# Optimization experiments

Measured on AMD Instinct MI355X. Metric: run time of the kernel, lower is better.

Reference implementation:

```python
import jax, jax.numpy as jnp
import numpy as np

B_, L_, OBS = 16, 1024, 64
H, NB, NST, DC, EXP = 256, 4, 16, 4, 2
DIN = EXP * H          # 512
DTR = (H + 15) // 16   # dt_rank = 16


def setup_inputs() -> dict:
    key = jax.random.key(0)
    ks = jax.random.split(key, 12)
    s = 0.02
    A_log = jnp.tile(jnp.log(jnp.arange(1, NST + 1, dtype=jnp.float32)), (NB, DIN, 1))
    return {
        "x": jax.random.normal(ks[0], (B_, L_, OBS), jnp.float32),
        "proj_w": jax.random.normal(ks[1], (H, OBS), jnp.float32) * s,
        "proj_b": jnp.zeros((H,), jnp.float32),
        "in_proj_w": jax.random.normal(ks[2], (NB, 2 * DIN, H), jnp.float32) * s,
        "conv_w": jax.random.normal(ks[3], (NB, DIN, DC), jnp.float32) * s,
        "conv_b": jnp.zeros((NB, DIN), jnp.float32),
        "x_proj_w": jax.random.normal(ks[4], (NB, DTR + 2 * NST, DIN), jnp.float32) * s,
        "dt_proj_w": jax.random.normal(ks[5], (NB, DIN, DTR), jnp.float32) * s,
        "dt_proj_b": jax.random.normal(ks[6], (NB, DIN), jnp.float32) * 0.1 - 3.0,
        "A_log": A_log,
        "D_skip": jnp.ones((NB, DIN), jnp.float32),
        "out_proj_w": jax.random.normal(ks[7], (NB, H, DIN), jnp.float32) * s,
        "head_w": jax.random.normal(ks[8], (1, H), jnp.float32) * s,
        "head_b": jnp.zeros((1,), jnp.float32),
    }


def _mamba(x, ipw, cw, cb, xpw, dpw, dpb, Alog, Dsk, opw):
    # x: [B, L, H]
    Bb, L, _ = x.shape
    xz = jnp.einsum('blh,eh->ble', x, ipw)           # [B,L,2*DIN]
    xin, z = jnp.split(xz, 2, axis=-1)
    # causal depthwise conv1d
    xc = jnp.transpose(xin, (0, 2, 1))               # [B,DIN,L]
    xc = jax.lax.conv_general_dilated(
        xc, cw[:, None, :], (1,), [(DC - 1, 0)],
        dimension_numbers=('NCH', 'OIH', 'NCH'), feature_group_count=DIN)
    u = jax.nn.silu(jnp.transpose(xc + cb[None, :, None], (0, 2, 1)))  # [B,L,DIN]
    # input-dependent dt, B, C
    proj = jnp.einsum('bld,ed->ble', u, xpw)         # [B,L,DTR+2*NST]
    dtl, Bc, Cc = jnp.split(proj, [DTR, DTR + NST], axis=-1)
    dt = jax.nn.softplus(jnp.einsum('blr,dr->bld', dtl, dpw) + dpb)     # [B,L,DIN]
    A = -jnp.exp(Alog)                               # [DIN,NST]

    def step(h, t):
        dt_t, B_t, C_t, u_t = t                      # [B,DIN],[B,NST],[B,NST],[B,DIN]
        h = jnp.exp(dt_t[:, :, None] * A) * h + (dt_t * u_t)[:, :, None] * B_t[:, None, :]
        return h, jnp.einsum('bdn,bn->bd', h, C_t)

    seq = (jnp.moveaxis(dt, 1, 0), jnp.moveaxis(Bc, 1, 0),
           jnp.moveaxis(Cc, 1, 0), jnp.moveaxis(u, 1, 0))
    h0 = jnp.zeros((Bb, DIN, NST), x.dtype)
    _, ys = jax.lax.scan(step, h0, seq)              # [L,B,DIN]
    y = jnp.moveaxis(ys, 0, 1) + Dsk * u
    y = y * jax.nn.silu(z)
    return jnp.einsum('bld,hd->blh', y, opw)


def reference(x, proj_w, proj_b, in_proj_w, conv_w, conv_b, x_proj_w,
              dt_proj_w, dt_proj_b, A_log, D_skip, out_proj_w, head_w, head_b):
    h = jnp.einsum('blo,ho->blh', x, proj_w) + proj_b
    for i in range(NB):
        h = _mamba(h, in_proj_w[i], conv_w[i], conv_b[i], x_proj_w[i],
                   dt_proj_w[i], dt_proj_b[i], A_log[i], D_skip[i], out_proj_w[i])
    v = jnp.einsum('bh,oh->bo', h[:, -1, :], head_w) + head_b  # [B,1]
    return v.squeeze(-1)
```

## Files before the change

### kernel.cpp

```cpp
#include <hip/hip_runtime.h>
#include <cstddef>

#define Bb 16
#define Ll 1024
#define OBS 64
#define Hh 256
#define NBLK 4
#define NST 16
#define DCV 4
#define DIN 512
#define DTR 16
#define NC 32
#define CL (Ll / NC)

typedef short short8 __attribute__((ext_vector_type(8)));
typedef float f32x4 __attribute__((ext_vector_type(4)));

#define LOG2E 1.4426950408889634f

#define HSZ ((size_t)Bb * Ll * Hh)
static const size_t OFF_XIN  = 2 * HSZ;
static const size_t OFF_Z    = OFF_XIN + (size_t)Bb * Ll * DIN;
static const size_t OFF_U    = OFF_Z   + (size_t)Bb * Ll * DIN;
static const size_t OFF_PROJ = OFF_U   + (size_t)Bb * Ll * DIN;
static const size_t OFF_HST  = OFF_PROJ + (size_t)Bb * Ll * 48;
static const size_t OFF_SDT  = OFF_HST + (size_t)Bb * NC * NST * DIN;
static const size_t OFF_WC   = OFF_SDT + (size_t)Bb * NC * DIN;
static const size_t WPW_HI  = 0;
static const size_t WPW_LO  = 16384;
static const size_t WIPW_HI = 32768;
static const size_t WIPW_LO = WIPW_HI + 1048576;
static const size_t WOPW_HI = WIPW_LO + 1048576;
static const size_t WOPW_LO = WOPW_HI + 524288;

__device__ inline unsigned short f32_to_bf16(float v) {
    unsigned int u = __float_as_uint(v);
    u += 0x7fffu + ((u >> 16) & 1u);
    return (unsigned short)(u >> 16);
}
__device__ inline float bf16_to_f32(unsigned short h) {
    return __uint_as_float((unsigned int)h << 16);
}
__device__ inline float softplusf(float s) {
    return fmaxf(s, 0.f) + log1pf(__expf(-fabsf(s)));
}
__device__ inline float fexp2(float x) { return __builtin_amdgcn_exp2f(x); }
__device__ inline void gload16(const void* g, void* l) {
    __builtin_amdgcn_global_load_lds(
        (const __attribute__((address_space(1))) void*)g,
        (__attribute__((address_space(3))) void*)l, 16, 0, 0);
}

__global__ __launch_bounds__(256) void convert_w_kernel(
    const float* __restrict__ w,
    unsigned short* __restrict__ hi,
    unsigned short* __restrict__ lo, int n4)
{
    int i = blockIdx.x * 256 + threadIdx.x;
    if (i >= n4) return;
    float4 v4 = ((const float4*)w)[i];
    float vv[4] = {v4.x, v4.y, v4.z, v4.w};
#pragma unroll
    for (int e = 0; e < 4; ++e) {
        unsigned short hb = f32_to_bf16(vv[e]);
        float res = vv[e] - bf16_to_f32(hb);
        hi[i * 4 + e] = hb;
        lo[i * 4 + e] = f32_to_bf16(res);
    }
}

template <int BM, int WR, int OUT>
__global__ __launch_bounds__(256) void gemm_bs(
    const unsigned short* __restrict__ Ahi,
    const unsigned short* __restrict__ Alo, int lda,
    const unsigned short* __restrict__ Whi,
    const unsigned short* __restrict__ Wlo,
    const float* __restrict__ bias,
    float* __restrict__ C0, float* __restrict__ C1,
    int nbx, int N, int K, int splitN)
{
    constexpr int WC_ = 4 / WR;
    constexpr int MI = (BM / WR) / 16;
    constexpr int NJ = (128 / WC_) / 16;
    constexpr int ASL = BM * 4 / 256;

    __shared__ unsigned short AsH[BM * 32], AsL[BM * 32];
    __shared__ unsigned short BsH[128 * 32], BsL[128 * 32];

    const int tid  = threadIdx.x;
    const int lane = tid & 63;
    const int w    = tid >> 6;
    const int wr   = w / WC_;
    const int wc   = w % WC_;

    const int swz = (blockIdx.x & 7) * (gridDim.x >> 3) + (blockIdx.x >> 3);
    const int m0 = (swz / nbx) * BM;
    const int n0 = (swz % nbx) * 128;

    f32x4 acc[MI][NJ] = {};

    for (int k0 = 0; k0 < K; k0 += 32) {
#pragma unroll
        for (int sI = 0; sI < ASL; ++sI) {
            int s = tid + sI * 256;
            int row = s >> 2, kb = s & 3;
            int kb2 = kb ^ ((row >> 1) & 3);
            size_t go = (size_t)(m0 + row) * lda + k0 + kb2 * 8;
            gload16(Ahi + go, &AsH[s * 8]);
            gload16(Alo + go, &AsL[s * 8]);
        }
#pragma unroll
        for (int sI = 0; sI < 2; ++sI) {
            int s = tid + sI * 256;
            int row = s >> 2, kb = s & 3;
            int kb2 = kb ^ ((row >> 1) & 3);
            size_t go = (size_t)(n0 + row) * K + k0 + kb2 * 8;
            gload16(Whi + go, &BsH[s * 8]);
            gload16(Wlo + go, &BsL[s * 8]);
        }
        __syncthreads();

        const int rr = lane & 15;
        const int kq = lane >> 4;
        short8 ah[MI], al[MI];
#pragma unroll
        for (int i = 0; i < MI; ++i) {
            int row = wr * (BM / WR) + i * 16 + rr;
            int off = row * 32 + (kq ^ ((row >> 1) & 3)) * 8;
            ah[i] = *(const short8*)&AsH[off];
            al[i] = *(const short8*)&AsL[off];
        }
#pragma unroll
        for (int j = 0; j < NJ; ++j) {
            int col = wc * (128 / WC_) + j * 16 + rr;
            int off = col * 32 + (kq ^ ((col >> 1) & 3)) * 8;
            short8 bh = *(const short8*)&BsH[off];
            short8 bl = *(const short8*)&BsL[off];
#pragma unroll
            for (int i = 0; i < MI; ++i) {
                acc[i][j] = __builtin_amdgcn_mfma_f32_16x16x32_bf16(ah[i], bh, acc[i][j], 0, 0, 0);
                acc[i][j] = __builtin_amdgcn_mfma_f32_16x16x32_bf16(ah[i], bl, acc[i][j], 0, 0, 0);
                acc[i][j] = __builtin_amdgcn_mfma_f32_16x16x32_bf16(al[i], bh, acc[i][j], 0, 0, 0);
            }
        }
        __syncthreads();
    }

    const int rr = lane & 15;
    const int rq = lane >> 4;
    unsigned short* Hd = (unsigned short*)C0;
    unsigned short* Ld = (unsigned short*)C1;
#pragma unroll
    for (int i = 0; i < MI; ++i) {
#pragma unroll
        for (int j = 0; j < NJ; ++j) {
            int col = n0 + wc * (128 / WC_) + j * 16 + rr;
            float badd = bias ? bias[col] : 0.f;
#pragma unroll
            for (int r = 0; r < 4; ++r) {
                int row = m0 + wr * (BM / WR) + i * 16 + rq * 4 + r;
                float v = acc[i][j][r] + badd;
                if (OUT == 0) {
                    if (col < splitN)
                        C0[(size_t)row * splitN + col] = v;
                    else
                        C1[(size_t)row * (N - splitN) + (col - splitN)] = v;
                } else {
                    unsigned short hb = f32_to_bf16(v);
                    Hd[(size_t)row * N + col] = hb;
                    Ld[(size_t)row * N + col] = f32_to_bf16(v - bf16_to_f32(hb));
                }
            }
        }
    }
}

template <int BM, int WR, int OUT>
__global__ __launch_bounds__(256) void gemm_mfma3(
    const float* __restrict__ A, int lda,
    const unsigned short* __restrict__ Whi,
    const unsigned short* __restrict__ Wlo,
    const float* __restrict__ bias,
    float* __restrict__ C0, float* __restrict__ C1,
    int nbx, int N, int K, int splitN)
{
    constexpr int WC_ = 4 / WR;
    constexpr int MI = (BM / WR) / 16;
    constexpr int NJ = (128 / WC_) / 16;
    constexpr int ASL = BM * 4 / 256;

    __shared__ unsigned short AsH[BM * 32], AsL[BM * 32];
    __shared__ unsigned short BsH[128 * 32], BsL[128 * 32];

    const int tid  = threadIdx.x;
    const int lane = tid & 63;
    const int w    = tid >> 6;
    const int wr   = w / WC_;
    const int wc   = w % WC_;

    const int swz = (blockIdx.x & 7) * (gridDim.x >> 3) + (blockIdx.x >> 3);
    const int m0 = (swz / nbx) * BM;
    const int n0 = (swz % nbx) * 128;

    f32x4 acc[MI][NJ] = {};

    for (int k0 = 0; k0 < K; k0 += 32) {
#pragma unroll
        for (int sI = 0; sI < 2; ++sI) {
            int s = tid + sI * 256;
            int row = s >> 2, kb = s & 3;
            int kb2 = kb ^ ((row >> 1) & 3);
            size_t go = (size_t)(n0 + row) * K + k0 + kb2 * 8;
            gload16(Whi + go, &BsH[s * 8]);
            gload16(Wlo + go, &BsL[s * 8]);
        }
#pragma unroll
        for (int sI = 0; sI < ASL; ++sI) {
            int s = tid + sI * 256;
            int row = s >> 2, kb = s & 3;
            int kb2 = kb ^ ((row >> 1) & 3);
            const float* ap = A + (size_t)(m0 + row) * lda + k0 + kb * 8;
            float4 v0 = *(const float4*)ap;
            float4 v1 = *(const float4*)(ap + 4);
            float vv[8] = {v0.x, v0.y, v0.z, v0.w, v1.x, v1.y, v1.z, v1.w};
            short8 h8, l8;
#pragma unroll
            for (int e = 0; e < 8; ++e) {
                unsigned short hb = f32_to_bf16(vv[e]);
                float res = vv[e] - bf16_to_f32(hb);
                h8[e] = (short)hb;
                l8[e] = (short)f32_to_bf16(res);
            }
            *(short8*)&AsH[row * 32 + kb2 * 8] = h8;
            *(short8*)&AsL[row * 32 + kb2 * 8] = l8;
        }
        __syncthreads();

        const int rr = lane & 15;
        const int kq = lane >> 4;
        short8 ah[MI], al[MI];
#pragma unroll
        for (int i = 0; i < MI; ++i) {
            int row = wr * (BM / WR) + i * 16 + rr;
            int off = row * 32 + (kq ^ ((row >> 1) & 3)) * 8;
            ah[i] = *(const short8*)&AsH[off];
            al[i] = *(const short8*)&AsL[off];
        }
#pragma unroll
        for (int j = 0; j < NJ; ++j) {
            int col = wc * (128 / WC_) + j * 16 + rr;
            int off = col * 32 + (kq ^ ((col >> 1) & 3)) * 8;
            short8 bh = *(const short8*)&BsH[off];
            short8 bl = *(const short8*)&BsL[off];
#pragma unroll
            for (int i = 0; i < MI; ++i) {
                acc[i][j] = __builtin_amdgcn_mfma_f32_16x16x32_bf16(ah[i], bh, acc[i][j], 0, 0, 0);
                acc[i][j] = __builtin_amdgcn_mfma_f32_16x16x32_bf16(ah[i], bl, acc[i][j], 0, 0, 0);
                acc[i][j] = __builtin_amdgcn_mfma_f32_16x16x32_bf16(al[i], bh, acc[i][j], 0, 0, 0);
            }
        }
        __syncthreads();
    }

    const int rr = lane & 15;
    const int rq = lane >> 4;
    unsigned short* Hd = (unsigned short*)C0;
    unsigned short* Ld = (unsigned short*)C1;
#pragma unroll
    for (int i = 0; i < MI; ++i) {
#pragma unroll
        for (int j = 0; j < NJ; ++j) {
            int col = n0 + wc * (128 / WC_) + j * 16 + rr;
            float badd = bias ? bias[col] : 0.f;
#pragma unroll
            for (int r = 0; r < 4; ++r) {
                int row = m0 + wr * (BM / WR) + i * 16 + rq * 4 + r;
                float v = acc[i][j][r] + badd;
                if (OUT == 0) {
                    if (col < splitN)
                        C0[(size_t)row * splitN + col] = v;
                    else
                        C1[(size_t)row * (N - splitN) + (col - splitN)] = v;
                } else {
                    unsigned short hb = f32_to_bf16(v);
                    Hd[(size_t)row * N + col] = hb;
                    Ld[(size_t)row * N + col] = f32_to_bf16(v - bf16_to_f32(hb));
                }
            }
        }
    }
}

template <int ACT>
__global__ __launch_bounds__(256) void gemm_nt(
    const float* __restrict__ A, int lda,
    const float* __restrict__ W,
    const float* __restrict__ bias,
    float* __restrict__ C0, float* __restrict__ C1,
    int M, int N, int K, int splitN)
{
    __shared__ float As[16][68];
    __shared__ float Ws[16][68];

    const int tid = threadIdx.x;
    const int m0 = blockIdx.y * 64;
    const int n0 = blockIdx.x * 64;
    const int tx = tid & 15;
    const int ty = tid >> 4;
    const int r  = tid >> 2;
    const int kv = (tid & 3) * 4;

    float acc[4][4] = {};

    for (int k0 = 0; k0 < K; k0 += 16) {
        float4 a4;
        {
            const float* ap = A + (size_t)(m0 + r) * lda + (k0 + kv);
            a4 = *(const float4*)ap;
        }
        float4 w4 = make_float4(0.f, 0.f, 0.f, 0.f);
        if (n0 + r < N) {
            const float* wp = W + (size_t)(n0 + r) * K + (k0 + kv);
            w4 = *(const float4*)wp;
        }
        __syncthreads();
        As[kv + 0][r] = a4.x; As[kv + 1][r] = a4.y;
        As[kv + 2][r] = a4.z; As[kv + 3][r] = a4.w;
        Ws[kv + 0][r] = w4.x; Ws[kv + 1][r] = w4.y;
        Ws[kv + 2][r] = w4.z; Ws[kv + 3][r] = w4.w;
        __syncthreads();
#pragma unroll
        for (int kk = 0; kk < 16; ++kk) {
            float4 av = *(const float4*)&As[kk][ty * 4];
            float4 wv = *(const float4*)&Ws[kk][tx * 4];
            float am[4] = {av.x, av.y, av.z, av.w};
            float wn[4] = {wv.x, wv.y, wv.z, wv.w};
#pragma unroll
            for (int i = 0; i < 4; ++i)
#pragma unroll
                for (int j = 0; j < 4; ++j)
                    acc[i][j] += am[i] * wn[j];
        }
    }

#pragma unroll
    for (int i = 0; i < 4; ++i) {
        const int row = m0 + ty * 4 + i;
#pragma unroll
        for (int j = 0; j < 4; ++j) {
            const int col = n0 + tx * 4 + j;
            if (col >= N) continue;
            float v = acc[i][j];
            if (bias) v += bias[col];
            if (ACT == 1) v = softplusf(v);
            if (col < splitN)
                C0[(size_t)row * splitN + col] = v;
            else
                C1[(size_t)row * (N - splitN) + (col - splitN)] = v;
        }
    }
}

__global__ __launch_bounds__(256) void conv_silu_kernel(
    const float* __restrict__ xin,
    const float* __restrict__ cw,
    const float* __restrict__ cb,
    float* __restrict__ u, int total4)
{
    int i = blockIdx.x * 256 + threadIdx.x;
    if (i >= total4) return;
    int d4 = (i & (DIN / 4 - 1)) * 4;
    int bl = i >> 7;
    int l  = bl & (Ll - 1);

    float4 cb4 = *(const float4*)(cb + d4);
    float acc[4] = {cb4.x, cb4.y, cb4.z, cb4.w};
    float4 cw0 = *(const float4*)(cw + (d4 + 0) * 4);
    float4 cw1 = *(const float4*)(cw + (d4 + 1) * 4);
    float4 cw2 = *(const float4*)(cw + (d4 + 2) * 4);
    float4 cw3 = *(const float4*)(cw + (d4 + 3) * 4);
    const float* cwp[4] = {(const float*)&cw0, (const float*)&cw1,
                           (const float*)&cw2, (const float*)&cw3};
#pragma unroll
    for (int k = 0; k < DCV; ++k) {
        int ls = l - (DCV - 1) + k;
        if (ls >= 0) {
            float4 xv = *(const float4*)(xin + (size_t)(bl - (DCV - 1) + k) * DIN + d4);
            float xj[4] = {xv.x, xv.y, xv.z, xv.w};
#pragma unroll
            for (int j = 0; j < 4; ++j) acc[j] += xj[j] * cwp[j][k];
        }
    }
    float4 o;
    o.x = acc[0] / (1.f + __expf(-acc[0]));
    o.y = acc[1] / (1.f + __expf(-acc[1]));
    o.z = acc[2] / (1.f + __expf(-acc[2]));
    o.w = acc[3] / (1.f + __expf(-acc[3]));
    *(float4*)(u + (size_t)bl * DIN + d4) = o;
}

__global__ __launch_bounds__(256) void scan_chunk_reduce(
    const float* __restrict__ dt,
    const float* __restrict__ u,
    const float* __restrict__ proj,
    const float* __restrict__ Alog,
    float* __restrict__ F,
    float* __restrict__ SDT)
{
    const int tid  = threadIdx.x;
    const int lane = tid & 63;
    const int widx = blockIdx.x * 4 + (tid >> 6);
    const int ng = lane >> 5;
    const int dd = lane & 31;
    const int d32 = widx & 15;
    const int c   = (widx >> 4) & (NC - 1);
    const int b   = widx >> 9;
    const int d   = d32 * 32 + dd;
    const int nb  = ng * 8;

    float A2[8];
#pragma unroll
    for (int j = 0; j < 8; ++j) A2[j] = -LOG2E * __expf(Alog[d * NST + nb + j]);

    float h[8];
#pragma unroll
    for (int j = 0; j < 8; ++j) h[j] = 0.f;
    float sdt = 0.f;

    const int l0 = c * CL;
    for (int l = l0; l < l0 + CL; ++l) {
        size_t row = (size_t)b * Ll + l;
        float dtv = dt[row * DIN + d];
        float uv  = u[row * DIN + d];
        float du  = dtv * uv;
        sdt += dtv;
        const float* pr = proj + row * 48;
        float4 B0 = *(const float4*)(pr + DTR + nb);
        float4 B1 = *(const float4*)(pr + DTR + nb + 4);
        float Bn[8] = {B0.x, B0.y, B0.z, B0.w, B1.x, B1.y, B1.z, B1.w};
#pragma unroll
        for (int j = 0; j < 8; ++j) {
            float e = fexp2(dtv * A2[j]);
            h[j] = e * h[j] + du * Bn[j];
        }
    }

    size_t base = (((size_t)b * NC + c) * NST + nb) * DIN + d;
#pragma unroll
    for (int j = 0; j < 8; ++j) F[base + (size_t)j * DIN] = h[j];
    if (ng == 0) SDT[((size_t)b * NC + c) * DIN + d] = sdt;
}

__global__ __launch_bounds__(256) void scan_prefix(
    const float* __restrict__ F,
    const float* __restrict__ SDT,
    const float* __restrict__ Alog,
    float* __restrict__ HST)
{
    int gid = blockIdx.x * 256 + threadIdx.x;
    int d = gid & (DIN - 1);
    int n = (gid >> 9) & (NST - 1);
    int b = gid >> 13;

    const float A2 = -LOG2E * __expf(Alog[d * NST + n]);

    const size_t stride = (size_t)NST * DIN;
    size_t idx  = (((size_t)b * NC + 0) * NST + n) * DIN + d;
    size_t sidx = ((size_t)b * NC + 0) * DIN + d;

    float fc = F[idx], sc = SDT[sidx];
    float h = 0.f;
    for (int c = 0; c < NC; ++c) {
        float fn = 0.f, sn = 0.f;
        if (c + 1 < NC) {
            fn = F[idx + stride];
            sn = SDT[sidx + DIN];
        }
        HST[idx] = h;
        h = fexp2(A2 * sc) * h + fc;
        fc = fn; sc = sn;
        idx += stride; sidx += DIN;
    }
}

__global__ __launch_bounds__(256) void scan_rescan_gate(
    const float* __restrict__ dt,
    const float* __restrict__ u,
    const float* __restrict__ proj,
    const float* __restrict__ Alog,
    const float* __restrict__ Dsk,
    const float* __restrict__ z,
    const float* __restrict__ HST,
    float* __restrict__ g)
{
    const int tid  = threadIdx.x;
    const int lane = tid & 63;
    const int widx = blockIdx.x * 4 + (tid >> 6);
    const int ng = lane >> 5;
    const int dd = lane & 31;
    const int d32 = widx & 15;
    const int c   = (widx >> 4) & (NC - 1);
    const int b   = widx >> 9;
    const int d   = d32 * 32 + dd;
    const int nb  = ng * 8;

    float A2[8];
#pragma unroll
    for (int j = 0; j < 8; ++j) A2[j] = -LOG2E * __expf(Alog[d * NST + nb + j]);
    const float Dv = Dsk[d];

    float h[8];
    {
        size_t base = (((size_t)b * NC + c) * NST + nb) * DIN + d;
#pragma unroll
        for (int j = 0; j < 8; ++j) h[j] = HST[base + (size_t)j * DIN];
    }

    const int l0 = c * CL;
    for (int l = l0; l < l0 + CL; ++l) {
        size_t row = (size_t)b * Ll + l;
        float dtv = dt[row * DIN + d];
        float uv  = u[row * DIN + d];
        float du  = dtv * uv;
        const float* pr = proj + row * 48;
        float4 B0 = *(const float4*)(pr + DTR + nb);
        float4 B1 = *(const float4*)(pr + DTR + nb + 4);
        float4 C0 = *(const float4*)(pr + 2 * DTR + nb);
        float4 C1 = *(const float4*)(pr + 2 * DTR + nb + 4);
        float Bn[8] = {B0.x, B0.y, B0.z, B0.w, B1.x, B1.y, B1.z, B1.w};
        float Cn[8] = {C0.x, C0.y, C0.z, C0.w, C1.x, C1.y, C1.z, C1.w};
        float y = 0.f;
#pragma unroll
        for (int j = 0; j < 8; ++j) {
            float e = fexp2(dtv * A2[j]);
            h[j] = e * h[j] + du * Bn[j];
            y += h[j] * Cn[j];
        }
        y += __shfl_xor(y, 32);
        if (ng == 0) {
            float zv = z[row * DIN + d];
            float sig = zv / (1.f + __expf(-zv));
            g[row * DIN + d] = (y + Dv * uv) * sig;
        }
    }
}

__global__ void head_kernel(const unsigned short* __restrict__ hhi,
                            const unsigned short* __restrict__ hlo,
                            const float* __restrict__ hw,
                            const float* __restrict__ hb,
                            float* __restrict__ out)
{
    int b = blockIdx.x;
    int t = threadIdx.x;
    const size_t base = ((size_t)b * Ll + (Ll - 1)) * Hh;
    float s = 0.f;
    for (int j = t; j < Hh; j += 64)
        s += (bf16_to_f32(hhi[base + j]) + bf16_to_f32(hlo[base + j])) * hw[j];
#pragma unroll
    for (int off = 32; off; off >>= 1) s += __shfl_down(s, off);
    if (t == 0) out[b] = s + hb[0];
}

extern "C" void kernel_launch(void* const* d_in, const int* in_sizes, int n_in,
                              void* d_out, int out_size, void* d_ws, size_t ws_size,
                              hipStream_t stream)
{
    const float* x    = (const float*)d_in[0];
    const float* pw   = (const float*)d_in[1];
    const float* pb   = (const float*)d_in[2];
    const float* ipw  = (const float*)d_in[3];
    const float* cw   = (const float*)d_in[4];
    const float* cb   = (const float*)d_in[5];
    const float* xpw  = (const float*)d_in[6];
    const float* dpw  = (const float*)d_in[7];
    const float* dpb  = (const float*)d_in[8];
    const float* Alog = (const float*)d_in[9];
    const float* Dsk  = (const float*)d_in[10];
    const float* opw  = (const float*)d_in[11];
    const float* hw   = (const float*)d_in[12];
    const float* hb   = (const float*)d_in[13];
    float* out = (float*)d_out;
    float* ws  = (float*)d_ws;

    float* hreg[2] = { ws, ws + HSZ };
    unsigned short* h_hi[2] = { (unsigned short*)hreg[0], (unsigned short*)hreg[1] };
    unsigned short* h_lo[2] = { h_hi[0] + HSZ, h_hi[1] + HSZ };

    float* xin  = ws + OFF_XIN;
    float* zb   = ws + OFF_Z;
    float* ub   = ws + OFF_U;
    float* prj  = ws + OFF_PROJ;
    float* hst  = ws + OFF_HST;
    float* sdt  = ws + OFF_SDT;
    float* dtb  = xin;
    unsigned short* wc = (unsigned short*)(ws + OFF_WC);

    const int M = Bb * Ll;
    const int SCAN_BLOCKS = Bb * NC * (DIN / 32) / 4;

    convert_w_kernel<<<(Hh * OBS / 4 + 255) / 256, 256, 0, stream>>>(
        pw, wc + WPW_HI, wc + WPW_LO, Hh * OBS / 4);
    convert_w_kernel<<<(NBLK * 2 * DIN * Hh / 4 + 255) / 256, 256, 0, stream>>>(
        ipw, wc + WIPW_HI, wc + WIPW_LO, NBLK * 2 * DIN * Hh / 4);
    convert_w_kernel<<<(NBLK * Hh * DIN / 4 + 255) / 256, 256, 0, stream>>>(
        opw, wc + WOPW_HI, wc + WOPW_LO, NBLK * Hh * DIN / 4);

    gemm_mfma3<64, 1, 1><<<dim3((Hh / 128) * (M / 64)), 256, 0, stream>>>(
        x, OBS, wc + WPW_HI, wc + WPW_LO, pb,
        (float*)h_hi[0], (float*)h_lo[0], Hh / 128, Hh, OBS, Hh);

    int cur = 0;
    for (int i = 0; i < NBLK; ++i) {
        const unsigned short* ipwh = wc + WIPW_HI + (size_t)i * 2 * DIN * Hh;
        const unsigned short* ipwl = wc + WIPW_LO + (size_t)i * 2 * DIN * Hh;
        const unsigned short* opwh = wc + WOPW_HI + (size_t)i * Hh * DIN;
        const unsigned short* opwl = wc + WOPW_LO + (size_t)i * Hh * DIN;
        const float* cw_i  = cw  + (size_t)i * DIN * DCV;
        const float* cb_i  = cb  + (size_t)i * DIN;
        const float* xpw_i = xpw + (size_t)i * 48 * DIN;
        const float* dpw_i = dpw + (size_t)i * DIN * DTR;
        const float* dpb_i = dpb + (size_t)i * DIN;
        const float* Al_i  = Alog + (size_t)i * DIN * NST;
        const float* Dk_i  = Dsk + (size_t)i * DIN;

        gemm_bs<128, 2, 0><<<dim3((2 * DIN / 128) * (M / 128)), 256, 0, stream>>>(
            h_hi[cur], h_lo[cur], Hh, ipwh, ipwl, nullptr,
            xin, zb, 2 * DIN / 128, 2 * DIN, Hh, DIN);

        conv_silu_kernel<<<(M * DIN / 4) / 256, 256, 0, stream>>>(
            xin, cw_i, cb_i, ub, M * DIN / 4);

        gemm_nt<0><<<dim3(1, M / 64), 256, 0, stream>>>(
            ub, DIN, xpw_i, nullptr, prj, nullptr, M, 48, DIN, 48);

        gemm_nt<1><<<dim3(DIN / 64, M / 64), 256, 0, stream>>>(
            prj, 48, dpw_i, dpb_i, dtb, nullptr, M, DIN, DTR, DIN);

        float* Fbuf = hreg[cur ^ 1];
        scan_chunk_reduce<<<SCAN_BLOCKS, 256, 0, stream>>>(
            dtb, ub, prj, Al_i, Fbuf, sdt);
        scan_prefix<<<(Bb * NST * DIN) / 256, 256, 0, stream>>>(
            Fbuf, sdt, Al_i, hst);
        scan_rescan_gate<<<SCAN_BLOCKS, 256, 0, stream>>>(
            dtb, ub, prj, Al_i, Dk_i, zb, hst, ub);

        gemm_mfma3<64, 1, 1><<<dim3((Hh / 128) * (M / 64)), 256, 0, stream>>>(
            ub, DIN, opwh, opwl, nullptr,
            (float*)h_hi[cur ^ 1], (float*)h_lo[cur ^ 1], Hh / 128, Hh, DIN, Hh);

        cur ^= 1;
    }

    head_kernel<<<Bb, 64, 0, stream>>>(h_hi[cur], h_lo[cur], hw, hb, out);
}
```

Before: 1.002 ms.

## Fuse dt projection and softplus into scan kernels via LDS recompute

Removes the separate dt_proj GEMM that wrote a full [B,L,DIN] dt tensor. Each scan block now loads the chunk's 16-wide dt_low rows into shared memory and computes softplus(dt_low·W + b) for its 128 channels into LDS. The scan loops then read dt from LDS instead of global memory. This cuts a kernel launch and the global dt write plus two reads, at the cost of computing dt twice (once in each scan kernel) and adding LDS usage and a block-wide sync.

```diff
diff --git a/kernel.cpp b/kernel.cpp
--- a/kernel.cpp
+++ b/kernel.cpp
@@ -399,24 +399,63 @@
     *(float4*)(u + (size_t)bl * DIN + d4) = o;
 }
 
+__device__ inline void build_dt_lds(
+    const float* __restrict__ proj, const float* __restrict__ dpw,
+    const float* __restrict__ dpb, size_t crow0, int d32_0, int tid,
+    float (*dtl)[16], float (*dts)[128])
+{
+    if (tid < 128) {
+        int row = tid >> 2, c4 = (tid & 3) * 4;
+        *(float4*)&dtl[row][c4] = *(const float4*)(proj + (crow0 + row) * 48 + c4);
+    }
+    __syncthreads();
+    const int dd = tid & 127;
+    const int d  = d32_0 * 32 + dd;
+    float wdt[16];
+    *(float4*)&wdt[0]  = *(const float4*)(dpw + d * DTR + 0);
+    *(float4*)&wdt[4]  = *(const float4*)(dpw + d * DTR + 4);
+    *(float4*)&wdt[8]  = *(const float4*)(dpw + d * DTR + 8);
+    *(float4*)&wdt[12] = *(const float4*)(dpw + d * DTR + 12);
+    const float bdt = dpb[d];
+#pragma unroll
+    for (int k = 0; k < 16; ++k) {
+        int l = (tid >> 7) + 2 * k;
+        const float* t = dtl[l];
+        float s = bdt;
+#pragma unroll
+        for (int r = 0; r < 16; ++r) s += t[r] * wdt[r];
+        dts[l][dd] = softplusf(s);
+    }
+    __syncthreads();
+}
+
 __global__ __launch_bounds__(256) void scan_chunk_reduce(
-    const float* __restrict__ dt,
     const float* __restrict__ u,
     const float* __restrict__ proj,
+    const float* __restrict__ dpw,
+    const float* __restrict__ dpb,
     const float* __restrict__ Alog,
     float* __restrict__ F,
     float* __restrict__ SDT)
 {
+    __shared__ float dtl[CL][16];
+    __shared__ float dts[CL][128];
+
     const int tid  = threadIdx.x;
     const int lane = tid & 63;
-    const int widx = blockIdx.x * 4 + (tid >> 6);
+    const int w    = tid >> 6;
+    const int widx0 = blockIdx.x * 4;
+    const int d32_0 = widx0 & 15;
+    const int c    = (widx0 >> 4) & (NC - 1);
+    const int b    = widx0 >> 9;
+    const size_t crow0 = (size_t)b * Ll + c * CL;
+
+    build_dt_lds(proj, dpw, dpb, crow0, d32_0, tid, dtl, dts);
+
     const int ng = lane >> 5;
-    const int dd = lane & 31;
-    const int d32 = widx & 15;
-    const int c   = (widx >> 4) & (NC - 1);
-    const int b   = widx >> 9;
-    const int d   = d32 * 32 + dd;
-    const int nb  = ng * 8;
+    const int ddw = w * 32 + (lane & 31);
+    const int d  = d32_0 * 32 + ddw;
+    const int nb = ng * 8;
 
     float A2[8];
 #pragma unroll
@@ -427,10 +466,9 @@
     for (int j = 0; j < 8; ++j) h[j] = 0.f;
     float sdt = 0.f;
 
-    const int l0 = c * CL;
-    for (int l = l0; l < l0 + CL; ++l) {
-        size_t row = (size_t)b * Ll + l;
-        float dtv = dt[row * DIN + d];
+    for (int l = 0; l < CL; ++l) {
+        size_t row = crow0 + l;
+        float dtv = dts[l][ddw];
         float uv  = u[row * DIN + d];
         float du  = dtv * uv;
         sdt += dtv;
@@ -484,25 +522,34 @@
 }
 
 __global__ __launch_bounds__(256) void scan_rescan_gate(
-    const float* __restrict__ dt,
     const float* __restrict__ u,
     const float* __restrict__ proj,
+    const float* __restrict__ dpw,
+    const float* __restrict__ dpb,
     const float* __restrict__ Alog,
     const float* __restrict__ Dsk,
     const float* __restrict__ z,
     const float* __restrict__ HST,
     float* __restrict__ g)
 {
+    __shared__ float dtl[CL][16];
+    __shared__ float dts[CL][128];
+
     const int tid  = threadIdx.x;
     const int lane = tid & 63;
-    const int widx = blockIdx.x * 4 + (tid >> 6);
+    const int w    = tid >> 6;
+    const int widx0 = blockIdx.x * 4;
+    const int d32_0 = widx0 & 15;
+    const int c    = (widx0 >> 4) & (NC - 1);
+    const int b    = widx0 >> 9;
+    const size_t crow0 = (size_t)b * Ll + c * CL;
+
+    build_dt_lds(proj, dpw, dpb, crow0, d32_0, tid, dtl, dts);
+
     const int ng = lane >> 5;
-    const int dd = lane & 31;
-    const int d32 = widx & 15;
-    const int c   = (widx >> 4) & (NC - 1);
-    const int b   = widx >> 9;
-    const int d   = d32 * 32 + dd;
-    const int nb  = ng * 8;
+    const int ddw = w * 32 + (lane & 31);
+    const int d  = d32_0 * 32 + ddw;
+    const int nb = ng * 8;
 
     float A2[8];
 #pragma unroll
@@ -516,10 +563,9 @@
         for (int j = 0; j < 8; ++j) h[j] = HST[base + (size_t)j * DIN];
     }
 
-    const int l0 = c * CL;
-    for (int l = l0; l < l0 + CL; ++l) {
-        size_t row = (size_t)b * Ll + l;
-        float dtv = dt[row * DIN + d];
+    for (int l = 0; l < CL; ++l) {
+        size_t row = crow0 + l;
+        float dtv = dts[l][ddw];
         float uv  = u[row * DIN + d];
         float du  = dtv * uv;
         const float* pr = proj + row * 48;
@@ -593,7 +639,6 @@
     float* prj  = ws + OFF_PROJ;
     float* hst  = ws + OFF_HST;
     float* sdt  = ws + OFF_SDT;
-    float* dtb  = xin;
     unsigned short* wc = (unsigned short*)(ws + OFF_WC);
 
     const int M = Bb * Ll;
@@ -634,16 +679,13 @@
         gemm_nt<0><<<dim3(1, M / 64), 256, 0, stream>>>(
             ub, DIN, xpw_i, nullptr, prj, nullptr, M, 48, DIN, 48);
 
-        gemm_nt<1><<<dim3(DIN / 64, M / 64), 256, 0, stream>>>(
-            prj, 48, dpw_i, dpb_i, dtb, nullptr, M, DIN, DTR, DIN);
-
         float* Fbuf = hreg[cur ^ 1];
         scan_chunk_reduce<<<SCAN_BLOCKS, 256, 0, stream>>>(
-            dtb, ub, prj, Al_i, Fbuf, sdt);
+            ub, prj, dpw_i, dpb_i, Al_i, Fbuf, sdt);
         scan_prefix<<<(Bb * NST * DIN) / 256, 256, 0, stream>>>(
             Fbuf, sdt, Al_i, hst);
         scan_rescan_gate<<<SCAN_BLOCKS, 256, 0, stream>>>(
-            dtb, ub, prj, Al_i, Dk_i, zb, hst, ub);
+            ub, prj, dpw_i, dpb_i, Al_i, Dk_i, zb, hst, ub);
 
         gemm_mfma3<64, 1, 1><<<dim3((Hh / 128) * (M / 64)), 256, 0, stream>>>(
             ub, DIN, opwh, opwl, nullptr,
```

Result: slower. 1.115 ms (+11.3%).
